# Kernel optimization log

Measured on AMD Instinct MI355X. Metric: run time of the kernel, lower is better.

The kernel has to match this reference:

```python
import jax, jax.numpy as jnp
import numpy as np

NUM_EXPERTS = 3
INPUT_DIM = 1024
HIDDEN_DIM = 4096
OUTPUT_DIM = 1024
ROUTER_HIDDEN = 128
BATCH = 8192


def setup_inputs() -> dict:
    key = jax.random.key(0)
    ks = jax.random.split(key, 6)
    s_in = 1.0 / np.sqrt(INPUT_DIM)
    s_h = 1.0 / np.sqrt(HIDDEN_DIM)
    s_rh = 1.0 / np.sqrt(ROUTER_HIDDEN)
    return {
        "x": jax.random.normal(ks[0], (BATCH, INPUT_DIM), jnp.float32),
        "router_w1": jax.random.normal(ks[1], (INPUT_DIM, ROUTER_HIDDEN), jnp.float32) * s_in,
        "router_b1": jnp.zeros((ROUTER_HIDDEN,), jnp.float32),
        "router_w2": jax.random.normal(ks[2], (ROUTER_HIDDEN, NUM_EXPERTS), jnp.float32) * s_rh,
        "router_b2": jnp.zeros((NUM_EXPERTS,), jnp.float32),
        "expert_w1": jax.random.normal(ks[3], (NUM_EXPERTS, INPUT_DIM, HIDDEN_DIM), jnp.float32) * s_in,
        "expert_b1": jnp.zeros((NUM_EXPERTS, HIDDEN_DIM), jnp.float32),
        "expert_w2": jax.random.normal(ks[4], (NUM_EXPERTS, HIDDEN_DIM, OUTPUT_DIM), jnp.float32) * s_h,
        "expert_b2": jnp.zeros((NUM_EXPERTS, OUTPUT_DIM), jnp.float32),
    }


def reference(x, router_w1, router_b1, router_w2, router_b2,
              expert_w1, expert_b1, expert_w2, expert_b2):
    # Router: MLP -> softmax probs, hard top-1 selection (argmax)
    rh = jax.nn.relu(x @ router_w1 + router_b1)          # [B, 128]
    logits = rh @ router_w2 + router_b2                   # [B, E]
    probs = jax.nn.softmax(logits, axis=-1)
    selected = jnp.argmax(probs, axis=-1)                 # [B] int

    # Per-expert forward on all tokens (dense equivalent of masked dispatch)
    h = jax.nn.relu(jnp.einsum('bi,eih->ebh', x, expert_w1) + expert_b1[:, None, :])  # [E,B,H]
    y = jnp.einsum('ebh,eho->ebo', h, expert_w2) + expert_b2[:, None, :]              # [E,B,O]

    # Scatter-combine: each token takes its selected expert's output
    outputs = jnp.take_along_axis(
        y, selected[None, :, None], axis=0)[0]            # [B, O]

    # routing_stats: tokens per expert
    routing_stats = jnp.bincount(selected, length=NUM_EXPERTS)
    return outputs, routing_stats
```

## Files before the change

### kernel.cpp

```cpp
#include <hip/hip_runtime.h>
#include <hip/hip_bf16.h>

typedef short bf16x8 __attribute__((ext_vector_type(8)));
typedef float f32x4 __attribute__((ext_vector_type(4)));
typedef __attribute__((address_space(1))) const void gconst_t;
typedef __attribute__((address_space(3))) void lds_t;

#define DEVI __device__ __forceinline__

constexpr int BATCH   = 8192;
constexpr int IN_DIM  = 1024;
constexpr int HID     = 4096;
constexpr int OUT_DIM = 1024;
constexpr int NE      = 3;

constexpr size_t XBF_OFF  = 0;
constexpr size_t W1T_OFF  = 16777216;
constexpr size_t W2T_OFF  = W1T_OFF + 25165824;
constexpr size_t H_OFF    = W2T_OFF + 25165824;
constexpr size_t XLO_OFF  = H_OFF;
constexpr size_t RHP_OFF  = H_OFF + 16777216;
constexpr size_t META_OFF = H_OFF + 67108864;
constexpr size_t W3_OFF   = META_OFF + 131072;

DEVI unsigned short f2bf(float f) {
  __hip_bfloat16 h = __float2bfloat16(f);
  return *reinterpret_cast<unsigned short*>(&h);
}
DEVI float bf2f(unsigned short u) {
  unsigned v = (unsigned)u << 16;
  return __uint_as_float(v);
}

DEVI unsigned swz(unsigned b) { return b ^ (((b >> 7) & 7u) << 4); }

__global__ __launch_bounds__(256) void prep_all(
    const float* __restrict__ x, const float* __restrict__ rw1,
    const float* __restrict__ ew1, const float* __restrict__ ew2,
    unsigned short* __restrict__ xb, unsigned short* __restrict__ xlo,
    unsigned short* __restrict__ w3, unsigned short* __restrict__ w1t,
    unsigned short* __restrict__ w2t) {
  __shared__ float tile[64][65];
  const int b = blockIdx.x;
  const int tid = threadIdx.x;
  if (b < 512) {
    const float4* xv4 = (const float4*)x;
    const int total = BATCH * IN_DIM / 4;
    for (int i = b * 256 + tid; i < total; i += 512 * 256) {
      const float4 v = xv4[i];
      ushort4 h, l;
      h.x = f2bf(v.x); l.x = f2bf(v.x - bf2f(h.x));
      h.y = f2bf(v.y); l.y = f2bf(v.y - bf2f(h.y));
      h.z = f2bf(v.z); l.z = f2bf(v.z - bf2f(h.z));
      h.w = f2bf(v.w); l.w = f2bf(v.w - bf2f(h.w));
      ((ushort4*)xb)[i] = h;
      ((ushort4*)xlo)[i] = l;
    }
  } else if (b < 544) {
    const int w = b - 512;
    const int r0 = (w >> 1) * 64;
    const int c0 = (w & 1) * 64;
    const int tr = tid >> 4;
    const int tc = (tid & 15) << 2;
#pragma unroll
    for (int i = 0; i < 4; i++) {
      const int r = tr + i * 16;
      const float4 v = *(const float4*)(rw1 + (size_t)(r0 + r) * 128 + (c0 + tc));
      tile[r][tc + 0] = v.x; tile[r][tc + 1] = v.y; tile[r][tc + 2] = v.z; tile[r][tc + 3] = v.w;
    }
    __syncthreads();
#pragma unroll
    for (int i = 0; i < 4; i++) {
      const int c = tr + i * 16;
      ushort4 hi, lo;
      {
        float f;
        f = tile[tc + 0][c]; hi.x = f2bf(f); lo.x = f2bf(f - bf2f(hi.x));
        f = tile[tc + 1][c]; hi.y = f2bf(f); lo.y = f2bf(f - bf2f(hi.y));
        f = tile[tc + 2][c]; hi.z = f2bf(f); lo.z = f2bf(f - bf2f(hi.z));
        f = tile[tc + 3][c]; hi.w = f2bf(f); lo.w = f2bf(f - bf2f(hi.w));
      }
      unsigned short* base = w3 + (size_t)(c0 + c) * 3072 + (r0 + tc);
      *(ushort4*)(base)        = hi;
      *(ushort4*)(base + 1024) = hi;
      *(ushort4*)(base + 2048) = lo;
    }
  } else {
    const int bb = b - 544;
    const float* src; unsigned short* dst; int R, C, r0, c0;
    if (bb < 3072) {
      const int e = bb / 1024, w = bb % 1024;
      src = ew1 + (size_t)e * 1024 * 4096; dst = w1t + (size_t)e * 4096 * 1024;
      R = 1024; C = 4096; r0 = (w & 15) * 64; c0 = (w >> 4) * 64;
    } else {
      const int b2 = bb - 3072, e = b2 / 1024, w = b2 % 1024;
      src = ew2 + (size_t)e * 4096 * 1024; dst = w2t + (size_t)e * 1024 * 4096;
      R = 4096; C = 1024; r0 = (w & 63) * 64; c0 = (w >> 6) * 64;
    }
    const int tr = tid >> 4;
    const int tc = (tid & 15) << 2;
#pragma unroll
    for (int i = 0; i < 4; i++) {
      const int r = tr + i * 16;
      const float4 v = *(const float4*)(src + (size_t)(r0 + r) * C + (c0 + tc));
      tile[r][tc + 0] = v.x; tile[r][tc + 1] = v.y; tile[r][tc + 2] = v.z; tile[r][tc + 3] = v.w;
    }
    __syncthreads();
#pragma unroll
    for (int i = 0; i < 4; i++) {
      const int c = tr + i * 16;
      ushort4 o;
      o.x = f2bf(tile[tc + 0][c]);
      o.y = f2bf(tile[tc + 1][c]);
      o.z = f2bf(tile[tc + 2][c]);
      o.w = f2bf(tile[tc + 3][c]);
      *(ushort4*)(dst + (size_t)(c0 + c) * R + (r0 + tc)) = o;
    }
  }
}

__global__ __launch_bounds__(256) void router_part(
    const unsigned short* __restrict__ xhi, const unsigned short* __restrict__ xlo,
    const unsigned short* __restrict__ w3, float* __restrict__ rhpart) {
  __shared__ unsigned short At[128 * 64];
  __shared__ unsigned short Bt[128 * 64];
  const int tid = threadIdx.x;
  const int m0 = blockIdx.x * 128;
  const int seg = blockIdx.y;
  const unsigned short* Abase = (seg == 1) ? xlo : xhi;
  const int kcol0 = seg * 1024;

  const unsigned short* asrc[4];
  const unsigned short* bsrc[4];
  unsigned loff[4];
#pragma unroll
  for (int l = 0; l < 4; l++) {
    const unsigned o = l * 4096u + (unsigned)tid * 16u;
    const unsigned p = swz(o);
    const int row = (int)(o >> 7);
    const int kel = (int)((p & 127u) >> 1);
    loff[l] = o;
    asrc[l] = Abase + (size_t)(m0 + row) * 1024 + kel;
    bsrc[l] = w3 + (size_t)row * 3072 + kcol0 + kel;
  }

  f32x4 acc[4][4];
#pragma unroll
  for (int i = 0; i < 4; i++)
#pragma unroll
    for (int j = 0; j < 4; j++) acc[i][j] = {0.f, 0.f, 0.f, 0.f};

  const int lane = tid & 63;
  const int wave = tid >> 6;
  const int wm = (wave >> 1) * 64;
  const int wn = (wave & 1) * 64;
  const int fr = lane & 15;
  const int fc = lane >> 4;

  for (int t = 0; t < 16; ++t) {
    __syncthreads();
#pragma unroll
    for (int l = 0; l < 4; l++) {
      __builtin_amdgcn_global_load_lds((gconst_t*)(asrc[l] + t * 64),
                                       (lds_t*)((char*)At + loff[l]), 16, 0, 0);
      __builtin_amdgcn_global_load_lds((gconst_t*)(bsrc[l] + t * 64),
                                       (lds_t*)((char*)Bt + loff[l]), 16, 0, 0);
    }
    __syncthreads();
    bf16x8 af[2][4], bv[2][4];
#pragma unroll
    for (int ks = 0; ks < 2; ks++) {
#pragma unroll
      for (int m = 0; m < 4; m++) {
        const unsigned L = (unsigned)(wm + m * 16 + fr) * 128u + (unsigned)(ks * 64 + fc * 16);
        af[ks][m] = *(const bf16x8*)((const char*)At + swz(L));
      }
#pragma unroll
      for (int n = 0; n < 4; n++) {
        const unsigned L = (unsigned)(wn + n * 16 + fr) * 128u + (unsigned)(ks * 64 + fc * 16);
        bv[ks][n] = *(const bf16x8*)((const char*)Bt + swz(L));
      }
    }
#pragma unroll
    for (int ks = 0; ks < 2; ks++)
#pragma unroll
      for (int m = 0; m < 4; m++)
#pragma unroll
        for (int n = 0; n < 4; n++)
          acc[m][n] = __builtin_amdgcn_mfma_f32_16x16x32_bf16(af[ks][m], bv[ks][n], acc[m][n], 0, 0, 0);
  }

  const int crow = (lane >> 4) * 4;
  const int ccol = lane & 15;
  float* outp = rhpart + (size_t)seg * BATCH * 128;
#pragma unroll
  for (int mi = 0; mi < 4; mi++) {
#pragma unroll
    for (int r = 0; r < 4; r++) {
      const int tok = m0 + wm + mi * 16 + crow + r;
#pragma unroll
      for (int ni = 0; ni < 4; ni++)
        outp[(size_t)tok * 128 + (wn + ni * 16 + ccol)] = acc[mi][ni][r];
    }
  }
}

__global__ __launch_bounds__(256) void router_finish(
    const float* __restrict__ rhpart, const float* __restrict__ rb1,
    const float* __restrict__ rw2, const float* __restrict__ rb2,
    int* __restrict__ counts, int* __restrict__ toklist) {
  __shared__ float rh[128 * 132];
  __shared__ float lg[128 * 3];
  const int tid = threadIdx.x;
  const int t0 = blockIdx.x * 128;
  constexpr size_t SEG = (size_t)BATCH * 128;

  for (int i = tid; i < 128 * 32; i += 256) {
    const int tok = i >> 5;
    const int c4 = (i & 31) * 4;
    const size_t base = (size_t)(t0 + tok) * 128 + c4;
    const float4 a = *(const float4*)(rhpart + base);
    const float4 b = *(const float4*)(rhpart + SEG + base);
    const float4 c = *(const float4*)(rhpart + 2 * SEG + base);
    const float4 bb = *(const float4*)(rb1 + c4);
    rh[tok * 132 + c4 + 0] = fmaxf(a.x + b.x + c.x + bb.x, 0.f);
    rh[tok * 132 + c4 + 1] = fmaxf(a.y + b.y + c.y + bb.y, 0.f);
    rh[tok * 132 + c4 + 2] = fmaxf(a.z + b.z + c.z + bb.z, 0.f);
    rh[tok * 132 + c4 + 3] = fmaxf(a.w + b.w + c.w + bb.w, 0.f);
  }
  __syncthreads();
#pragma unroll
  for (int pass = 0; pass < 2; ++pass) {
    const int t = tid + pass * 256;
    if (t < 384) {
      const int tok = t / 3, e = t - tok * 3;
      float s = rb2[e];
#pragma unroll 4
      for (int j = 0; j < 128; ++j) s = fmaf(rh[tok * 132 + j], rw2[j * 3 + e], s);
      lg[tok * 3 + e] = s;
    }
  }
  __syncthreads();
  if (tid < 128) {
    const float l0 = lg[tid * 3], l1 = lg[tid * 3 + 1], l2 = lg[tid * 3 + 2];
    int sel = 0; float m = l0;
    if (l1 > m) { m = l1; sel = 1; }
    if (l2 > m) { m = l2; sel = 2; }
    const int slot = atomicAdd(&counts[sel], 1);
    toklist[sel * BATCH + slot] = t0 + tid;
  }
}

template <int MODE>
__global__ __launch_bounds__(256, 3) void moe_gemm(
    const unsigned short* __restrict__ Abase, const unsigned short* __restrict__ Ball,
    const float* __restrict__ biasAll, unsigned short* __restrict__ Hout,
    float* __restrict__ Yout, const int* __restrict__ toklist, const int* __restrict__ counts,
    float* __restrict__ tail) {
  constexpr int N  = (MODE == 0) ? HID : OUT_DIM;
  constexpr int K  = (MODE == 0) ? IN_DIM : HID;
  constexpr int NT = K / 32;

  const int tid = threadIdx.x;
  if (MODE == 0 && blockIdx.x == 0 && blockIdx.y == 0 && tid < NE)
    tail[tid] = (float)counts[tid];

  const int c0 = counts[0], c1 = counts[1], c2 = counts[2];
  const int mb0 = (c0 + 127) >> 7, mb1 = (c1 + 127) >> 7, mb2 = (c2 + 127) >> 7;
  const int bx = blockIdx.x;
  int e, mblk;
  if (bx < mb0) { e = 0; mblk = bx; }
  else if (bx < mb0 + mb1) { e = 1; mblk = bx - mb0; }
  else if (bx < mb0 + mb1 + mb2) { e = 2; mblk = bx - mb0 - mb1; }
  else return;
  const int cnt = (e == 0) ? c0 : (e == 1) ? c1 : c2;
  const int m0 = mblk * 128;
  const int n0 = blockIdx.y * 128;
  const int off_e = (e > 0 ? c0 : 0) + (e > 1 ? c1 : 0);
  const unsigned short* Bmat = Ball + (size_t)e * ((size_t)N * K);
  const float* bias = biasAll + (size_t)e * N;

  __shared__ unsigned short Ab[3][128 * 32];
  __shared__ unsigned short Bb[3][128 * 32];

  const unsigned short* asrc[2];
  const unsigned short* bsrc[2];
  unsigned aoff[2], boff[2];
#pragma unroll
  for (int l = 0; l < 2; l++) {
    const unsigned o = l * 4096u + (unsigned)tid * 16u;
    const unsigned p = o ^ (((o >> 6) & 3u) << 4);
    const int row = (int)(o >> 6);
    const int kel = (int)((p & 63u) >> 1);
    aoff[l] = o;
    boff[l] = o;
    int slot = m0 + row; if (slot > cnt - 1) slot = cnt - 1;
    const size_t arow = (MODE == 0) ? (size_t)toklist[e * BATCH + slot]
                                    : (size_t)(off_e + slot);
    asrc[l] = Abase + arow * K + kel;
    bsrc[l] = Bmat + (size_t)(n0 + row) * K + kel;
  }

  f32x4 acc[4][4];
#pragma unroll
  for (int i = 0; i < 4; i++)
#pragma unroll
    for (int j = 0; j < 4; j++) acc[i][j] = {0.f, 0.f, 0.f, 0.f};

  const int lane = tid & 63;
  const int wave = tid >> 6;
  const int wm = (wave >> 1) * 64;
  const int wn = (wave & 1) * 64;
  const int fr = lane & 15;
  const int fc = lane >> 4;

  auto STAGE = [&](int buf, int kofs) {
#pragma unroll
    for (int l = 0; l < 2; l++)
      __builtin_amdgcn_global_load_lds((gconst_t*)(asrc[l] + kofs),
                                       (lds_t*)((char*)&Ab[buf][0] + aoff[l]), 16, 0, 0);
#pragma unroll
    for (int l = 0; l < 2; l++)
      __builtin_amdgcn_global_load_lds((gconst_t*)(bsrc[l] + kofs),
                                       (lds_t*)((char*)&Bb[buf][0] + boff[l]), 16, 0, 0);
  };

  STAGE(0, 0);
  STAGE(1, 32);

  int cur = 0;
  for (int t = 0; t < NT; ++t) {
    if (t + 1 < NT) asm volatile("s_waitcnt vmcnt(4)" ::: "memory");
    else            asm volatile("s_waitcnt vmcnt(0)" ::: "memory");
    __builtin_amdgcn_sched_barrier(0);
    __builtin_amdgcn_s_barrier();
    __builtin_amdgcn_sched_barrier(0);
    bf16x8 af[4], bv[4];
#pragma unroll
    for (int m = 0; m < 4; m++) {
      const unsigned row = (unsigned)(wm + m * 16 + fr);
      const unsigned addr = ((row << 6) + (unsigned)(fc << 4)) ^ ((row & 3u) << 4);
      af[m] = *(const bf16x8*)((const char*)&Ab[cur][0] + addr);
    }
#pragma unroll
    for (int n = 0; n < 4; n++) {
      const unsigned row = (unsigned)(wn + n * 16 + fr);
      const unsigned addr = ((row << 6) + (unsigned)(fc << 4)) ^ ((row & 3u) << 4);
      bv[n] = *(const bf16x8*)((const char*)&Bb[cur][0] + addr);
    }
    asm volatile("s_waitcnt lgkmcnt(0)" ::: "memory");
    __builtin_amdgcn_sched_barrier(0);
    __builtin_amdgcn_s_setprio(1);
#pragma unroll
    for (int m = 0; m < 4; m++)
#pragma unroll
      for (int n = 0; n < 4; n++)
        acc[m][n] = __builtin_amdgcn_mfma_f32_16x16x32_bf16(af[m], bv[n], acc[m][n], 0, 0, 0);
    __builtin_amdgcn_s_setprio(0);
    if (t + 2 < NT) {
      const int nb = (cur + 2 >= 3) ? cur - 1 : cur + 2;
      STAGE(nb, (t + 2) * 32);
    }
    cur = (cur + 1 == 3) ? 0 : cur + 1;
  }

  const int crow = (lane >> 4) * 4;
  const int ccol = lane & 15;
#pragma unroll
  for (int mi = 0; mi < 4; mi++) {
#pragma unroll
    for (int r = 0; r < 4; r++) {
      const int slot = m0 + wm + mi * 16 + crow + r;
      if (slot >= cnt) continue;
      if (MODE == 0) {
        unsigned short* hrow = Hout + (size_t)(off_e + slot) * HID;
#pragma unroll
        for (int ni = 0; ni < 4; ni++) {
          const int n = n0 + wn + ni * 16 + ccol;
          const float v = acc[mi][ni][r] + bias[n];
          hrow[n] = f2bf(fmaxf(v, 0.f));
        }
      } else {
        const int tok = toklist[e * BATCH + slot];
        float* yrow = Yout + (size_t)tok * OUT_DIM;
#pragma unroll
        for (int ni = 0; ni < 4; ni++) {
          const int n = n0 + wn + ni * 16 + ccol;
          yrow[n] = acc[mi][ni][r] + bias[n];
        }
      }
    }
  }
}

extern "C" void kernel_launch(void* const* d_in, const int* in_sizes, int n_in,
                              void* d_out, int out_size, void* d_ws, size_t ws_size,
                              hipStream_t stream) {
  const float* x   = (const float*)d_in[0];
  const float* rw1 = (const float*)d_in[1];
  const float* rb1 = (const float*)d_in[2];
  const float* rw2 = (const float*)d_in[3];
  const float* rb2 = (const float*)d_in[4];
  const float* ew1 = (const float*)d_in[5];
  const float* eb1 = (const float*)d_in[6];
  const float* ew2 = (const float*)d_in[7];
  const float* eb2 = (const float*)d_in[8];
  float* out = (float*)d_out;

  char* ws = (char*)d_ws;
  unsigned short* xb  = (unsigned short*)(ws + XBF_OFF);
  unsigned short* w1t = (unsigned short*)(ws + W1T_OFF);
  unsigned short* w2t = (unsigned short*)(ws + W2T_OFF);
  unsigned short* h   = (unsigned short*)(ws + H_OFF);
  unsigned short* xlo = (unsigned short*)(ws + XLO_OFF);
  float* rhpart = (float*)(ws + RHP_OFF);
  int* counts  = (int*)(ws + META_OFF);
  int* toklist = counts + 16;
  unsigned short* w3 = (unsigned short*)(ws + W3_OFF);
  float* tail = out + (size_t)BATCH * OUT_DIM;

  hipMemsetAsync(counts, 0, 64, stream);
  prep_all<<<6688, 256, 0, stream>>>(x, rw1, ew1, ew2, xb, xlo, w3, w1t, w2t);
  router_part<<<dim3(64, 3), 256, 0, stream>>>(xb, xlo, w3, rhpart);
  router_finish<<<64, 256, 0, stream>>>(rhpart, rb1, rw2, rb2, counts, toklist);
  moe_gemm<0><<<dim3(66, 32), 256, 0, stream>>>(xb, w1t, eb1, h, nullptr, toklist, counts, tail);
  moe_gemm<1><<<dim3(66, 8), 256, 0, stream>>>(h, w2t, eb2, nullptr, out, toklist, counts, tail);
}
```

Measured before the change: 371.8 us.

## Enlarge MoE GEMM tiles to 256x256x64 with 8 waves and phased prefetch

Rewrites the grouped expert GEMM to use 256x256 output tiles with a K step of 64 and 512 threads (8 waves, each computing 128x64). LDS buffering moves from a 3-stage 32-wide ring to a double buffer of 64-wide tiles. Next-tile global-to-LDS loads are split into four pairs interleaved with four compute phases, each with its own barrier and waitcnt. The aim is higher arithmetic intensity per byte loaded and fewer blocks, at the cost of far fewer concurrent blocks per CU (occupancy), more barriers, and more padding waste on partial expert M-tiles.

```diff
diff --git a/kernel.cpp b/kernel.cpp
--- a/kernel.cpp
+++ b/kernel.cpp
@@ -252,21 +252,21 @@
 }
 
 template <int MODE>
-__global__ __launch_bounds__(256, 3) void moe_gemm(
+__global__ __launch_bounds__(512) void moe_gemm(
     const unsigned short* __restrict__ Abase, const unsigned short* __restrict__ Ball,
     const float* __restrict__ biasAll, unsigned short* __restrict__ Hout,
     float* __restrict__ Yout, const int* __restrict__ toklist, const int* __restrict__ counts,
     float* __restrict__ tail) {
   constexpr int N  = (MODE == 0) ? HID : OUT_DIM;
   constexpr int K  = (MODE == 0) ? IN_DIM : HID;
-  constexpr int NT = K / 32;
+  constexpr int NT = K / 64;
 
   const int tid = threadIdx.x;
   if (MODE == 0 && blockIdx.x == 0 && blockIdx.y == 0 && tid < NE)
     tail[tid] = (float)counts[tid];
 
   const int c0 = counts[0], c1 = counts[1], c2 = counts[2];
-  const int mb0 = (c0 + 127) >> 7, mb1 = (c1 + 127) >> 7, mb2 = (c2 + 127) >> 7;
+  const int mb0 = (c0 + 255) >> 8, mb1 = (c1 + 255) >> 8, mb2 = (c2 + 255) >> 8;
   const int bx = blockIdx.x;
   int e, mblk;
   if (bx < mb0) { e = 0; mblk = bx; }
@@ -274,100 +274,128 @@
   else if (bx < mb0 + mb1 + mb2) { e = 2; mblk = bx - mb0 - mb1; }
   else return;
   const int cnt = (e == 0) ? c0 : (e == 1) ? c1 : c2;
-  const int m0 = mblk * 128;
-  const int n0 = blockIdx.y * 128;
+  const int m0 = mblk * 256;
+  const int n0 = blockIdx.y * 256;
   const int off_e = (e > 0 ? c0 : 0) + (e > 1 ? c1 : 0);
   const unsigned short* Bmat = Ball + (size_t)e * ((size_t)N * K);
   const float* bias = biasAll + (size_t)e * N;
 
-  __shared__ unsigned short Ab[3][128 * 32];
-  __shared__ unsigned short Bb[3][128 * 32];
-
-  const unsigned short* asrc[2];
-  const unsigned short* bsrc[2];
-  unsigned aoff[2], boff[2];
-#pragma unroll
-  for (int l = 0; l < 2; l++) {
-    const unsigned o = l * 4096u + (unsigned)tid * 16u;
-    const unsigned p = o ^ (((o >> 6) & 3u) << 4);
-    const int row = (int)(o >> 6);
-    const int kel = (int)((p & 63u) >> 1);
-    aoff[l] = o;
-    boff[l] = o;
+  __shared__ unsigned short Ab[2][256 * 64];
+  __shared__ unsigned short Bb[2][256 * 64];
+
+  const unsigned short* asrc[4];
+  const unsigned short* bsrc[4];
+  unsigned qoff[4];
+#pragma unroll
+  for (int q = 0; q < 4; q++) {
+    const unsigned ot = q * 8192u + (unsigned)tid * 16u;
+    const unsigned p = swz(ot);
+    const int row = (int)(ot >> 7);
+    const int kel = (int)((p & 127u) >> 1);
+    qoff[q] = ot;
     int slot = m0 + row; if (slot > cnt - 1) slot = cnt - 1;
     const size_t arow = (MODE == 0) ? (size_t)toklist[e * BATCH + slot]
                                     : (size_t)(off_e + slot);
-    asrc[l] = Abase + arow * K + kel;
-    bsrc[l] = Bmat + (size_t)(n0 + row) * K + kel;
-  }
-
-  f32x4 acc[4][4];
-#pragma unroll
-  for (int i = 0; i < 4; i++)
+    asrc[q] = Abase + arow * K + kel;
+    bsrc[q] = Bmat + (size_t)(n0 + row) * K + kel;
+  }
+
+  auto STG = [&](int pair, int buf, int t) {
+    const int kofs = t * 64;
+    if (pair == 0) {
+      __builtin_amdgcn_global_load_lds((gconst_t*)(bsrc[0] + kofs),
+                                       (lds_t*)((char*)&Bb[buf][0] + qoff[0]), 16, 0, 0);
+      __builtin_amdgcn_global_load_lds((gconst_t*)(bsrc[1] + kofs),
+                                       (lds_t*)((char*)&Bb[buf][0] + qoff[1]), 16, 0, 0);
+    } else if (pair == 1) {
+      __builtin_amdgcn_global_load_lds((gconst_t*)(bsrc[2] + kofs),
+                                       (lds_t*)((char*)&Bb[buf][0] + qoff[2]), 16, 0, 0);
+      __builtin_amdgcn_global_load_lds((gconst_t*)(bsrc[3] + kofs),
+                                       (lds_t*)((char*)&Bb[buf][0] + qoff[3]), 16, 0, 0);
+    } else if (pair == 2) {
+      __builtin_amdgcn_global_load_lds((gconst_t*)(asrc[0] + kofs),
+                                       (lds_t*)((char*)&Ab[buf][0] + qoff[0]), 16, 0, 0);
+      __builtin_amdgcn_global_load_lds((gconst_t*)(asrc[2] + kofs),
+                                       (lds_t*)((char*)&Ab[buf][0] + qoff[2]), 16, 0, 0);
+    } else {
+      __builtin_amdgcn_global_load_lds((gconst_t*)(asrc[1] + kofs),
+                                       (lds_t*)((char*)&Ab[buf][0] + qoff[1]), 16, 0, 0);
+      __builtin_amdgcn_global_load_lds((gconst_t*)(asrc[3] + kofs),
+                                       (lds_t*)((char*)&Ab[buf][0] + qoff[3]), 16, 0, 0);
+    }
+  };
+
+  f32x4 acc[8][4];
+#pragma unroll
+  for (int i = 0; i < 8; i++)
 #pragma unroll
     for (int j = 0; j < 4; j++) acc[i][j] = {0.f, 0.f, 0.f, 0.f};
 
   const int lane = tid & 63;
   const int wave = tid >> 6;
-  const int wm = (wave >> 1) * 64;
-  const int wn = (wave & 1) * 64;
+  const int wm = (wave >> 2) * 128;
+  const int wn = (wave & 3) * 64;
   const int fr = lane & 15;
   const int fc = lane >> 4;
 
-  auto STAGE = [&](int buf, int kofs) {
-#pragma unroll
-    for (int l = 0; l < 2; l++)
-      __builtin_amdgcn_global_load_lds((gconst_t*)(asrc[l] + kofs),
-                                       (lds_t*)((char*)&Ab[buf][0] + aoff[l]), 16, 0, 0);
-#pragma unroll
-    for (int l = 0; l < 2; l++)
-      __builtin_amdgcn_global_load_lds((gconst_t*)(bsrc[l] + kofs),
-                                       (lds_t*)((char*)&Bb[buf][0] + boff[l]), 16, 0, 0);
-  };
-
-  STAGE(0, 0);
-  STAGE(1, 32);
-
-  int cur = 0;
+  STG(0, 0, 0); STG(1, 0, 0); STG(2, 0, 0); STG(3, 0, 0);
+  asm volatile("s_waitcnt vmcnt(2)" ::: "memory");
+  __builtin_amdgcn_sched_barrier(0);
+  __builtin_amdgcn_s_barrier();
+
   for (int t = 0; t < NT; ++t) {
-    if (t + 1 < NT) asm volatile("s_waitcnt vmcnt(4)" ::: "memory");
-    else            asm volatile("s_waitcnt vmcnt(0)" ::: "memory");
-    __builtin_amdgcn_sched_barrier(0);
-    __builtin_amdgcn_s_barrier();
-    __builtin_amdgcn_sched_barrier(0);
-    bf16x8 af[4], bv[4];
-#pragma unroll
-    for (int m = 0; m < 4; m++) {
-      const unsigned row = (unsigned)(wm + m * 16 + fr);
-      const unsigned addr = ((row << 6) + (unsigned)(fc << 4)) ^ ((row & 3u) << 4);
-      af[m] = *(const bf16x8*)((const char*)&Ab[cur][0] + addr);
-    }
-#pragma unroll
-    for (int n = 0; n < 4; n++) {
-      const unsigned row = (unsigned)(wn + n * 16 + fr);
-      const unsigned addr = ((row << 6) + (unsigned)(fc << 4)) ^ ((row & 3u) << 4);
-      bv[n] = *(const bf16x8*)((const char*)&Bb[cur][0] + addr);
-    }
-    asm volatile("s_waitcnt lgkmcnt(0)" ::: "memory");
-    __builtin_amdgcn_sched_barrier(0);
-    __builtin_amdgcn_s_setprio(1);
-#pragma unroll
-    for (int m = 0; m < 4; m++)
-#pragma unroll
-      for (int n = 0; n < 4; n++)
-        acc[m][n] = __builtin_amdgcn_mfma_f32_16x16x32_bf16(af[m], bv[n], acc[m][n], 0, 0, 0);
-    __builtin_amdgcn_s_setprio(0);
-    if (t + 2 < NT) {
-      const int nb = (cur + 2 >= 3) ? cur - 1 : cur + 2;
-      STAGE(nb, (t + 2) * 32);
-    }
-    cur = (cur + 1 == 3) ? 0 : cur + 1;
+    const int cur = t & 1;
+    const bool more = (t + 1 < NT);
+    const char* Ac = (const char*)&Ab[cur][0];
+    const char* Bc = (const char*)&Bb[cur][0];
+#pragma unroll
+    for (int ph = 0; ph < 4; ++ph) {
+      bf16x8 af[2][2], bv[2][4];
+#pragma unroll
+      for (int ks = 0; ks < 2; ks++) {
+#pragma unroll
+        for (int mm = 0; mm < 2; mm++) {
+          const unsigned L = (unsigned)(wm + (2 * ph + mm) * 16 + fr) * 128u +
+                             (unsigned)(ks * 64 + fc * 16);
+          af[ks][mm] = *(const bf16x8*)(Ac + swz(L));
+        }
+#pragma unroll
+        for (int nn = 0; nn < 4; nn++) {
+          const unsigned L = (unsigned)(wn + nn * 16 + fr) * 128u +
+                             (unsigned)(ks * 64 + fc * 16);
+          bv[ks][nn] = *(const bf16x8*)(Bc + swz(L));
+        }
+      }
+      if (more) STG(ph, cur ^ 1, t + 1);
+      if (ph == 1) {
+        if (more) asm volatile("s_waitcnt vmcnt(4)" ::: "memory");
+        else      asm volatile("s_waitcnt vmcnt(0)" ::: "memory");
+        __builtin_amdgcn_sched_barrier(0);
+      } else if (ph == 3 && more) {
+        asm volatile("s_waitcnt vmcnt(2)" ::: "memory");
+        __builtin_amdgcn_sched_barrier(0);
+      }
+      __builtin_amdgcn_s_barrier();
+      asm volatile("s_waitcnt lgkmcnt(0)" ::: "memory");
+      __builtin_amdgcn_sched_barrier(0);
+      __builtin_amdgcn_s_setprio(1);
+#pragma unroll
+      for (int ks = 0; ks < 2; ks++)
+#pragma unroll
+        for (int mm = 0; mm < 2; mm++)
+#pragma unroll
+          for (int nn = 0; nn < 4; nn++)
+            acc[2 * ph + mm][nn] = __builtin_amdgcn_mfma_f32_16x16x32_bf16(
+                af[ks][mm], bv[ks][nn], acc[2 * ph + mm][nn], 0, 0, 0);
+      __builtin_amdgcn_s_setprio(0);
+      __builtin_amdgcn_s_barrier();
+    }
   }
 
   const int crow = (lane >> 4) * 4;
   const int ccol = lane & 15;
 #pragma unroll
-  for (int mi = 0; mi < 4; mi++) {
+  for (int mi = 0; mi < 8; mi++) {
 #pragma unroll
     for (int r = 0; r < 4; r++) {
       const int slot = m0 + wm + mi * 16 + crow + r;
@@ -423,6 +451,6 @@
   prep_all<<<6688, 256, 0, stream>>>(x, rw1, ew1, ew2, xb, xlo, w3, w1t, w2t);
   router_part<<<dim3(64, 3), 256, 0, stream>>>(xb, xlo, w3, rhpart);
   router_finish<<<64, 256, 0, stream>>>(rhpart, rb1, rw2, rb2, counts, toklist);
-  moe_gemm<0><<<dim3(66, 32), 256, 0, stream>>>(xb, w1t, eb1, h, nullptr, toklist, counts, tail);
-  moe_gemm<1><<<dim3(66, 8), 256, 0, stream>>>(h, w2t, eb2, nullptr, out, toklist, counts, tail);
-}
+  moe_gemm<0><<<dim3(34, 16), 512, 0, stream>>>(xb, w1t, eb1, h, nullptr, toklist, counts, tail);
+  moe_gemm<1><<<dim3(34, 4), 512, 0, stream>>>(h, w2t, eb2, nullptr, out, toklist, counts, tail);
+}
```

Result: slower. 408.8 us (+9.9%).
